# Kernel optimization log

Hardware: AMD Instinct MI355X
Metric: run time of the kernel (lower is better)

The kernel has to match this reference:

```python
import jax, jax.numpy as jnp
import numpy as np

B = 16384
IN = 512
A = 16
E = 9  # 9 position-specific experts
H1, H2, H3 = 512, 256, 128


def setup_inputs() -> dict:
    key = jax.random.key(0)
    ks = jax.random.split(key, 10)
    s = lambda fan_in: 1.0 / np.sqrt(fan_in)
    return {
        "x": jax.random.normal(ks[0], (B, IN), dtype=jnp.float32),
        "position": jax.random.randint(ks[1], (B,), 0, 9, dtype=jnp.int64),
        # torch Linear convention: W [out, in], y = x @ W.T + b; stacked per expert [E, out, in]
        "W1": jax.random.uniform(ks[2], (E, H1, IN), jnp.float32, -s(IN), s(IN)),
        "b1": jax.random.uniform(ks[3], (E, H1), jnp.float32, -s(IN), s(IN)),
        "W2": jax.random.uniform(ks[4], (E, H2, H1), jnp.float32, -s(H1), s(H1)),
        "b2": jax.random.uniform(ks[5], (E, H2), jnp.float32, -s(H1), s(H1)),
        "W3": jax.random.uniform(ks[6], (E, H3, H2), jnp.float32, -s(H2), s(H2)),
        "b3": jax.random.uniform(ks[7], (E, H3), jnp.float32, -s(H2), s(H2)),
        "W4": jax.random.uniform(ks[8], (E, A, H3), jnp.float32, -s(H3), s(H3)),
        "b4": jax.random.uniform(ks[9], (E, A), jnp.float32, -s(H3), s(H3)),
    }


def reference(x, position, W1, b1, W2, b2, W3, b3, W4, b4):
    # Each sample i is routed through expert min(position[i], 8).
    # Dense MoE reference: run all 9 experts over the full batch, then
    # select the routed expert's logits per sample (same math as the
    # per-sample Python loop in the original module).
    pos = jnp.minimum(position, 8)
    h = jax.nn.relu(jnp.einsum('bi,eoi->ebo', x, W1) + b1[:, None, :])   # [E,B,H1]
    h = jax.nn.relu(jnp.einsum('ebi,eoi->ebo', h, W2) + b2[:, None, :])  # [E,B,H2]
    h = jax.nn.relu(jnp.einsum('ebi,eoi->ebo', h, W3) + b3[:, None, :])  # [E,B,H3]
    logits_all = jnp.einsum('ebi,eoi->ebo', h, W4) + b4[:, None, :]      # [E,B,A]
    logits = logits_all[pos, jnp.arange(x.shape[0])]                     # [B,A]
    return jax.nn.softmax(logits, axis=1)
```

## Files before the change

### kernel.cpp

```cpp
#include <hip/hip_runtime.h>

typedef _Float16 f16;
typedef __attribute__((ext_vector_type(8))) _Float16 f16x8;
typedef __attribute__((ext_vector_type(4))) _Float16 f16x4;
typedef __attribute__((ext_vector_type(4))) float f32x4;

#define MFMA16(a, b, c) __builtin_amdgcn_mfma_f32_16x16x32_f16(a, b, c, 0, 0, 0)

#define B_N 16384
#define E_N 9
#define TILE 32
#define NTILE_MAX 520
#define THREADS 512

#define D_IN 512
#define D_H1 512
#define D_H2 256
#define D_H3 128
#define D_A 16

#define O1B 0
#define O2B 4718592
#define O3B 7077888
#define O4B 7667712
#define WPL_BYTES 7704576
#define WSLOTS (WPL_BYTES / 16)

#define IDX_OFF 64
#define WP_OFF 131584
#define WS_NEED (WP_OFF + (size_t)WPL_BYTES)

#define XS_OFF 0
#define H1_OFF 32768
#define H2_OFF 0
#define H3_OFF 16384
#define LDS_BYTES 65536


__global__ void k_bucket(const int* __restrict__ pos, int* __restrict__ hdr,
                         int* __restrict__ idx) {
  __shared__ int cnt[E_N], cur[E_N];
  __shared__ int flag_s;
  const int t = threadIdx.x;
  if (t < E_N) cnt[t] = 0;
  if (t == 0) {
    int nz = 0;
    for (int i = 0; i < 64; ++i) nz |= pos[2 * i + 1];
    flag_s = (nz == 0) ? 1 : 0;
  }
  __syncthreads();
  const bool f64 = flag_s != 0;
  int e[16];
#pragma unroll
  for (int k = 0; k < 16; ++k) {
    int i = k * 1024 + t;
    long long v = f64 ? ((const long long*)pos)[i] : (long long)pos[i];
    v = v < 0 ? 0 : (v > 8 ? 8 : v);
    e[k] = (int)v;
    atomicAdd(&cnt[e[k]], 1);
  }
  __syncthreads();
  if (t == 0) {
    int acc = 0;
    for (int ee = 0; ee < E_N; ++ee) { cur[ee] = acc; acc += cnt[ee]; }
  }
  if (t < E_N) hdr[8 + t] = cnt[t];
  __syncthreads();
#pragma unroll
  for (int k = 0; k < 16; ++k) {
    int i = k * 1024 + t;
    int slot = atomicAdd(&cur[e[k]], 1);
    idx[slot] = i;
  }
}


__global__ void k_wcvt(const float* __restrict__ W1, const float* __restrict__ W2,
                       const float* __restrict__ W3, const float* __restrict__ W4,
                       char* __restrict__ wp) {
  int slot = blockIdx.x * 256 + threadIdx.x;
  if (slot >= WSLOTS) return;
  long addr = (long)slot << 4;
  int lane = (int)((addr >> 4) & 63);
  int lg = lane >> 4, ln = lane & 15;
  const float* src;
  if (addr < O2B) {
    int rec = (int)(addr >> 10);
    int f = rec & 63, w = (rec >> 6) & 7, e = rec >> 9;
    int n = w * 64 + (f >> 5) * 32 + (f & 1) * 16 + ln;
    int k = ((f >> 2) & 7) * 64 + ((f >> 1) & 1) * 32 + lg * 8;
    src = W1 + ((long)e * D_H1 + n) * D_IN + k;
  } else if (addr < O3B) {
    int rec = (int)((addr - O2B) >> 10);
    int f = rec & 31, w = (rec >> 5) & 7, e = rec >> 8;
    int n = w * 32 + (f & 1) * 16 + ln;
    int k = (f >> 2) * 64 + ((f >> 1) & 1) * 32 + lg * 8;
    src = W2 + ((long)e * D_H2 + n) * D_H1 + k;
  } else if (addr < O4B) {
    int rec = (int)((addr - O3B) >> 10);
    int f = rec & 7, w = (rec >> 3) & 7, e = rec >> 6;
    int n = w * 16 + ln;
    int k = (f >> 1) * 64 + (f & 1) * 32 + lg * 8;
    src = W3 + ((long)e * D_H3 + n) * D_H2 + k;
  } else {
    long rel = addr - O4B;
    int e = (int)(rel >> 12);
    int r2 = (int)(rel & 4095);
    int s = r2 >> 4, n = s >> 4, k16 = s & 15;
    src = W4 + ((long)e * D_A + n) * D_H3 + k16 * 8;
  }
  float4 a = *(const float4*)src;
  float4 b = *(const float4*)(src + 4);
  f16x8 h;
  h[0] = (f16)a.x; h[1] = (f16)a.y; h[2] = (f16)a.z; h[3] = (f16)a.w;
  h[4] = (f16)b.x; h[5] = (f16)b.y; h[6] = (f16)b.z; h[7] = (f16)b.w;
  *(f16x8*)(wp + addr) = h;
}


__device__ __forceinline__ f16x8 afrag(const char* base, int strideB, int rowoff,
                                       int kbytes, int lane) {
  int m = rowoff + (lane & 15);
  int q = kbytes + ((lane >> 4) * 16);
  return *(const f16x8*)(base + m * strideB + (q ^ ((lane & 15) << 4)));
}

__device__ __forceinline__ void ldfrag4(f16x8* q, const char* wb, int f0, int lane) {
  const char* p = wb + (long)f0 * 1024 + lane * 16;
  q[0] = *(const f16x8*)(p);
  q[1] = *(const f16x8*)(p + 1024);
  q[2] = *(const f16x8*)(p + 2048);
  q[3] = *(const f16x8*)(p + 3072);
}
__device__ __forceinline__ void ldfrag2(f16x8* q, const char* wb, int f0, int lane) {
  const char* p = wb + (long)f0 * 1024 + lane * 16;
  q[0] = *(const f16x8*)(p);
  q[1] = *(const f16x8*)(p + 1024);
}

__launch_bounds__(THREADS, 4)
__global__ void k_mlp(const float* __restrict__ x,
                      const float* __restrict__ b1, const float* __restrict__ b2,
                      const float* __restrict__ b3, const float* __restrict__ b4,
                      const int* __restrict__ hdr, const int* __restrict__ idx,
                      const char* __restrict__ wp, float* __restrict__ out) {
  __shared__ __align__(16) char lds[LDS_BYTES];

  int b = blockIdx.x;
  int bswz = (b & 7) * (NTILE_MAX / 8) + (b >> 3);

  const int* counts = hdr + 8;
  int e = -1, tile = 0, base = 0, ne = 0;
  {
    int acc = 0, off = 0;
    for (int ee = 0; ee < E_N; ++ee) {
      int n = counts[ee];
      int nt = (n + TILE - 1) / TILE;
      if (bswz < acc + nt) { e = ee; tile = bswz - acc; ne = n; base = off; break; }
      acc += nt; off += n;
    }
  }
  if (e < 0) return;
  const int rvalid = min(TILE, ne - tile * TILE);
  const int row0 = base + tile * TILE;

  const int t = threadIdx.x;
  const int lane = t & 63;
  const int wid = t >> 6;
  const int lg = lane >> 4;
  const int ln = lane & 15;

  const char* wb1 = wp + O1B + (((long)e * 8 + wid) << 16);
  const char* wb2 = wp + O2B + (((long)e * 8 + wid) << 15);
  const char* wb3 = wp + O3B + (((long)e * 8 + wid) << 13);
  const char* wpe4 = wp + O4B + (long)e * 4096;

  f16x8 Q[3][4];
  ldfrag4(Q[0], wb1, 0, lane);
  ldfrag4(Q[1], wb1, 4, lane);

  const float4* x4 = (const float4*)x;
  for (int u = t; u < TILE * (D_IN / 4); u += THREADS) {
    int s = u >> 7, c4 = u & 127;
    float4 v = make_float4(0.f, 0.f, 0.f, 0.f);
    if (s < rvalid) v = x4[(long)idx[row0 + s] * (D_IN / 4) + c4];
    f16x4 h;
    h[0] = (f16)v.x; h[1] = (f16)v.y; h[2] = (f16)v.z; h[3] = (f16)v.w;
    *(f16x4*)(lds + XS_OFF + s * 1024 + ((c4 * 8) ^ ((s & 15) << 4))) = h;
  }
  __syncthreads();

  {
    f32x4 acc[2][2];
#pragma unroll
    for (int g = 0; g < 16; ++g) {
      if (g < 14) ldfrag4(Q[(g + 2) % 3], wb1, (g + 2) * 4, lane);
      const int kb = g & 7;
      if (kb == 0) {
#pragma unroll
        for (int m = 0; m < 2; ++m)
#pragma unroll
          for (int nf = 0; nf < 2; ++nf) acc[m][nf] = (f32x4){0.f, 0.f, 0.f, 0.f};
      }
      f16x8* cq = Q[g % 3];
      __builtin_amdgcn_s_setprio(1);
#pragma unroll
      for (int kc = 0; kc < 2; ++kc) {
        f16x8 A0 = afrag(lds + XS_OFF, 1024, 0, kb * 128 + kc * 64, lane);
        f16x8 A1 = afrag(lds + XS_OFF, 1024, 16, kb * 128 + kc * 64, lane);
        acc[0][0] = MFMA16(A0, cq[kc * 2 + 0], acc[0][0]);
        acc[0][1] = MFMA16(A0, cq[kc * 2 + 1], acc[0][1]);
        acc[1][0] = MFMA16(A1, cq[kc * 2 + 0], acc[1][0]);
        acc[1][1] = MFMA16(A1, cq[kc * 2 + 1], acc[1][1]);
      }
      __builtin_amdgcn_s_setprio(0);
      if (kb == 7) {
        const int nf32 = g >> 3;
#pragma unroll
        for (int nf = 0; nf < 2; ++nf) {
          int n = wid * 64 + nf32 * 32 + nf * 16 + ln;
          float bias = b1[e * D_H1 + n];
#pragma unroll
          for (int m = 0; m < 2; ++m)
#pragma unroll
            for (int j = 0; j < 4; ++j) {
              float v = acc[m][nf][j] + bias;
              v = v > 0.f ? v : 0.f;
              int rw = m * 16 + lg * 4 + j;
              *(f16*)(lds + H1_OFF + rw * 1024 + ((n * 2) ^ ((rw & 15) << 4))) = (f16)v;
            }
        }
      }
    }
  }
  __syncthreads();

  {
    ldfrag4(Q[0], wb2, 0, lane);
    ldfrag4(Q[1], wb2, 4, lane);
    f32x4 acc[2][2];
#pragma unroll
    for (int m = 0; m < 2; ++m)
#pragma unroll
      for (int nf = 0; nf < 2; ++nf) acc[m][nf] = (f32x4){0.f, 0.f, 0.f, 0.f};
#pragma unroll
    for (int g = 0; g < 8; ++g) {
      if (g < 6) ldfrag4(Q[(g + 2) % 3], wb2, (g + 2) * 4, lane);
      f16x8* cq = Q[g % 3];
      __builtin_amdgcn_s_setprio(1);
#pragma unroll
      for (int kc = 0; kc < 2; ++kc) {
        f16x8 A0 = afrag(lds + H1_OFF, 1024, 0, g * 128 + kc * 64, lane);
        f16x8 A1 = afrag(lds + H1_OFF, 1024, 16, g * 128 + kc * 64, lane);
        acc[0][0] = MFMA16(A0, cq[kc * 2 + 0], acc[0][0]);
        acc[0][1] = MFMA16(A0, cq[kc * 2 + 1], acc[0][1]);
        acc[1][0] = MFMA16(A1, cq[kc * 2 + 0], acc[1][0]);
        acc[1][1] = MFMA16(A1, cq[kc * 2 + 1], acc[1][1]);
      }
      __builtin_amdgcn_s_setprio(0);
    }
#pragma unroll
    for (int nf = 0; nf < 2; ++nf) {
      int n = wid * 32 + nf * 16 + ln;
      float bias = b2[e * D_H2 + n];
#pragma unroll
      for (int m = 0; m < 2; ++m)
#pragma unroll
        for (int j = 0; j < 4; ++j) {
          float v = acc[m][nf][j] + bias;
          v = v > 0.f ? v : 0.f;
          int rw = m * 16 + lg * 4 + j;
          *(f16*)(lds + H2_OFF + rw * 512 + ((n * 2) ^ ((rw & 15) << 4))) = (f16)v;
        }
    }
  }
  __syncthreads();

  {
    ldfrag2(Q[0], wb3, 0, lane);
    ldfrag2(Q[1], wb3, 2, lane);
    f32x4 acc3[2];
    acc3[0] = (f32x4){0.f, 0.f, 0.f, 0.f};
    acc3[1] = (f32x4){0.f, 0.f, 0.f, 0.f};
#pragma unroll
    for (int g = 0; g < 4; ++g) {
      if (g < 2) ldfrag2(Q[(g + 2) % 3], wb3, (g + 2) * 2, lane);
      f16x8* cq = Q[g % 3];
      __builtin_amdgcn_s_setprio(1);
#pragma unroll
      for (int kc = 0; kc < 2; ++kc) {
        f16x8 B0 = cq[kc];
#pragma unroll
        for (int m = 0; m < 2; ++m) {
          f16x8 A = afrag(lds + H2_OFF, 512, m * 16, g * 128 + kc * 64, lane);
          acc3[m] = MFMA16(A, B0, acc3[m]);
        }
      }
      __builtin_amdgcn_s_setprio(0);
    }
    int n = wid * 16 + ln;
    float bias = b3[e * D_H3 + n];
#pragma unroll
    for (int m = 0; m < 2; ++m)
#pragma unroll
      for (int j = 0; j < 4; ++j) {
        float v = acc3[m][j] + bias;
        v = v > 0.f ? v : 0.f;
        int rw = m * 16 + lg * 4 + j;
        *(f16*)(lds + H3_OFF + rw * 256 + ((n * 2) ^ ((rw & 15) << 4))) = (f16)v;
      }
  }
  __syncthreads();

  if (wid < 2) {
    f32x4 a4 = (f32x4){0.f, 0.f, 0.f, 0.f};
#pragma unroll
    for (int kc = 0; kc < 4; ++kc) {
      f16x8 Bv = *(const f16x8*)(wpe4 + ln * 256 + kc * 64 + lg * 16);
      f16x8 Av = afrag(lds + H3_OFF, 256, wid * 16, kc * 64, lane);
      a4 = MFMA16(Av, Bv, a4);
    }
    float bias = b4[e * D_A + ln];
#pragma unroll
    for (int j = 0; j < 4; ++j) {
      float v = a4[j] + bias;
      float mx = v;
      for (int msk = 8; msk >= 1; msk >>= 1) mx = fmaxf(mx, __shfl_xor(mx, msk));
      float pe = expf(v - mx);
      float sm = pe;
      for (int msk = 8; msk >= 1; msk >>= 1) sm += __shfl_xor(sm, msk);
      int rl = wid * 16 + lg * 4 + j;
      if (rl < rvalid) out[(long)idx[row0 + rl] * D_A + ln] = pe / sm;
    }
  }
}


extern "C" void kernel_launch(void* const* d_in, const int* in_sizes, int n_in,
                              void* d_out, int out_size, void* d_ws, size_t ws_size,
                              hipStream_t stream) {
  const float* x  = (const float*)d_in[0];
  const int* pos  = (const int*)d_in[1];
  const float* W1 = (const float*)d_in[2];
  const float* b1 = (const float*)d_in[3];
  const float* W2 = (const float*)d_in[4];
  const float* b2 = (const float*)d_in[5];
  const float* W3 = (const float*)d_in[6];
  const float* b3 = (const float*)d_in[7];
  const float* W4 = (const float*)d_in[8];
  const float* b4 = (const float*)d_in[9];
  float* out = (float*)d_out;

  int* hdr = (int*)d_ws;
  int* idx = hdr + IDX_OFF;
  char* wp = (char*)d_ws + WP_OFF;

  hipLaunchKernelGGL(k_bucket, dim3(1), dim3(1024), 0, stream, pos, hdr, idx);
  hipLaunchKernelGGL(k_wcvt, dim3(WSLOTS / 256), dim3(256), 0, stream,
                     W1, W2, W3, W4, wp);
  hipLaunchKernelGGL(k_mlp, dim3(NTILE_MAX), dim3(THREADS), 0, stream,
                     x, b1, b2, b3, b4, hdr, idx, wp, out);
}
```

Baseline: 64.06 us.

## Merge prep kernels, interleave per-warp weight layout, halve LDS for occupancy

Fuses the bucketing and weight-conversion kernels into a single launch, with block 0 doing the bucketing. The packed weights are relaid per expert and warp so that W1, W2 and W3 fragments for a warp sit contiguously, and they are streamed through a rolling 4-register prefetch instead of the old 3x4 buffer. Hidden activations are held in registers and written back into the reused input LDS region after a barrier, which halves LDS to 32KB, and launch bounds are raised to 8 blocks per CU. The cost is extra barriers and a shallower prefetch window, and the higher occupancy target may force register spills.

After: 89.00 us. 38.9% more time.

```diff
diff --git a/kernel.cpp b/kernel.cpp
--- a/kernel.cpp
+++ b/kernel.cpp
@@ -19,9 +19,7 @@
 #define D_H3 128
 #define D_A 16
 
-#define O1B 0
-#define O2B 4718592
-#define O3B 7077888
+#define RPW 104
 #define O4B 7667712
 #define WPL_BYTES 7704576
 #define WSLOTS (WPL_BYTES / 16)
@@ -31,77 +29,79 @@
 #define WS_NEED (WP_OFF + (size_t)WPL_BYTES)
 
 #define XS_OFF 0
-#define H1_OFF 32768
 #define H2_OFF 0
 #define H3_OFF 16384
-#define LDS_BYTES 65536
-
-
-__global__ void k_bucket(const int* __restrict__ pos, int* __restrict__ hdr,
-                         int* __restrict__ idx) {
-  __shared__ int cnt[E_N], cur[E_N];
-  __shared__ int flag_s;
-  const int t = threadIdx.x;
-  if (t < E_N) cnt[t] = 0;
-  if (t == 0) {
-    int nz = 0;
-    for (int i = 0; i < 64; ++i) nz |= pos[2 * i + 1];
-    flag_s = (nz == 0) ? 1 : 0;
-  }
-  __syncthreads();
-  const bool f64 = flag_s != 0;
-  int e[16];
-#pragma unroll
-  for (int k = 0; k < 16; ++k) {
-    int i = k * 1024 + t;
-    long long v = f64 ? ((const long long*)pos)[i] : (long long)pos[i];
-    v = v < 0 ? 0 : (v > 8 ? 8 : v);
-    e[k] = (int)v;
-    atomicAdd(&cnt[e[k]], 1);
-  }
-  __syncthreads();
-  if (t == 0) {
-    int acc = 0;
-    for (int ee = 0; ee < E_N; ++ee) { cur[ee] = acc; acc += cnt[ee]; }
-  }
-  if (t < E_N) hdr[8 + t] = cnt[t];
-  __syncthreads();
-#pragma unroll
-  for (int k = 0; k < 16; ++k) {
-    int i = k * 1024 + t;
-    int slot = atomicAdd(&cur[e[k]], 1);
-    idx[slot] = i;
-  }
-}
-
-
-__global__ void k_wcvt(const float* __restrict__ W1, const float* __restrict__ W2,
+#define LDS_BYTES 32768
+
+
+__global__ void k_prep(const int* __restrict__ pos,
+                       const float* __restrict__ W1, const float* __restrict__ W2,
                        const float* __restrict__ W3, const float* __restrict__ W4,
+                       int* __restrict__ hdr, int* __restrict__ idx,
                        char* __restrict__ wp) {
-  int slot = blockIdx.x * 256 + threadIdx.x;
+  if (blockIdx.x == 0) {
+    __shared__ int cnt[E_N], cur[E_N];
+    __shared__ int flag_s;
+    const int t = threadIdx.x;
+    if (t < E_N) cnt[t] = 0;
+    if (t == 0) {
+      int nz = 0;
+      for (int i = 0; i < 64; ++i) nz |= pos[2 * i + 1];
+      flag_s = (nz == 0) ? 1 : 0;
+    }
+    __syncthreads();
+    const bool f64 = flag_s != 0;
+#pragma unroll 4
+    for (int k = 0; k < 64; ++k) {
+      int i = k * 256 + t;
+      long long v = f64 ? ((const long long*)pos)[i] : (long long)pos[i];
+      v = v < 0 ? 0 : (v > 8 ? 8 : v);
+      atomicAdd(&cnt[(int)v], 1);
+    }
+    __syncthreads();
+    if (t == 0) {
+      int acc = 0;
+      for (int ee = 0; ee < E_N; ++ee) { cur[ee] = acc; acc += cnt[ee]; }
+    }
+    if (t < E_N) hdr[8 + t] = cnt[t];
+    __syncthreads();
+#pragma unroll 4
+    for (int k = 0; k < 64; ++k) {
+      int i = k * 256 + t;
+      long long v = f64 ? ((const long long*)pos)[i] : (long long)pos[i];
+      v = v < 0 ? 0 : (v > 8 ? 8 : v);
+      int slot = atomicAdd(&cur[(int)v], 1);
+      idx[slot] = i;
+    }
+    return;
+  }
+
+  int slot = (blockIdx.x - 1) * 256 + threadIdx.x;
   if (slot >= WSLOTS) return;
   long addr = (long)slot << 4;
-  int lane = (int)((addr >> 4) & 63);
+  int lane = slot & 63;
   int lg = lane >> 4, ln = lane & 15;
   const float* src;
-  if (addr < O2B) {
+  if (addr < O4B) {
     int rec = (int)(addr >> 10);
-    int f = rec & 63, w = (rec >> 6) & 7, e = rec >> 9;
-    int n = w * 64 + (f >> 5) * 32 + (f & 1) * 16 + ln;
-    int k = ((f >> 2) & 7) * 64 + ((f >> 1) & 1) * 32 + lg * 8;
-    src = W1 + ((long)e * D_H1 + n) * D_IN + k;
-  } else if (addr < O3B) {
-    int rec = (int)((addr - O2B) >> 10);
-    int f = rec & 31, w = (rec >> 5) & 7, e = rec >> 8;
-    int n = w * 32 + (f & 1) * 16 + ln;
-    int k = (f >> 2) * 64 + ((f >> 1) & 1) * 32 + lg * 8;
-    src = W2 + ((long)e * D_H2 + n) * D_H1 + k;
-  } else if (addr < O4B) {
-    int rec = (int)((addr - O3B) >> 10);
-    int f = rec & 7, w = (rec >> 3) & 7, e = rec >> 6;
-    int n = w * 16 + ln;
-    int k = (f >> 1) * 64 + (f & 1) * 32 + lg * 8;
-    src = W3 + ((long)e * D_H3 + n) * D_H2 + k;
+    int f = rec % RPW;
+    int ew = rec / RPW;
+    int w = ew & 7, e = ew >> 3;
+    if (f < 64) {
+      int n = w * 64 + ((f >> 5) & 1) * 32 + (f & 1) * 16 + ln;
+      int k = ((f >> 2) & 7) * 64 + ((f >> 1) & 1) * 32 + lg * 8;
+      src = W1 + ((long)e * D_H1 + n) * D_IN + k;
+    } else if (f < 96) {
+      int j = f - 64;
+      int n = w * 32 + (j & 1) * 16 + ln;
+      int k = (j >> 2) * 64 + ((j >> 1) & 1) * 32 + lg * 8;
+      src = W2 + ((long)e * D_H2 + n) * D_H1 + k;
+    } else {
+      int j = f - 96;
+      int n = w * 16 + ln;
+      int k = (j >> 1) * 64 + (j & 1) * 32 + lg * 8;
+      src = W3 + ((long)e * D_H3 + n) * D_H2 + k;
+    }
   } else {
     long rel = addr - O4B;
     int e = (int)(rel >> 12);
@@ -122,23 +122,14 @@
                                        int kbytes, int lane) {
   int m = rowoff + (lane & 15);
   int q = kbytes + ((lane >> 4) * 16);
-  return *(const f16x8*)(base + m * strideB + (q ^ ((lane & 15) << 4)));
-}
-
-__device__ __forceinline__ void ldfrag4(f16x8* q, const char* wb, int f0, int lane) {
-  const char* p = wb + (long)f0 * 1024 + lane * 16;
-  q[0] = *(const f16x8*)(p);
-  q[1] = *(const f16x8*)(p + 1024);
-  q[2] = *(const f16x8*)(p + 2048);
-  q[3] = *(const f16x8*)(p + 3072);
-}
-__device__ __forceinline__ void ldfrag2(f16x8* q, const char* wb, int f0, int lane) {
-  const char* p = wb + (long)f0 * 1024 + lane * 16;
-  q[0] = *(const f16x8*)(p);
-  q[1] = *(const f16x8*)(p + 1024);
-}
-
-__launch_bounds__(THREADS, 4)
+  return *(const f16x8*)(base + m * strideB + (q ^ ((m & 15) << 4)));
+}
+
+__device__ __forceinline__ f16x8 ldfrag(const char* wb, int f, int lane) {
+  return *(const f16x8*)(wb + (long)f * 1024 + lane * 16);
+}
+
+__launch_bounds__(THREADS, 8)
 __global__ void k_mlp(const float* __restrict__ x,
                       const float* __restrict__ b1, const float* __restrict__ b2,
                       const float* __restrict__ b3, const float* __restrict__ b4,
@@ -170,14 +161,14 @@
   const int lg = lane >> 4;
   const int ln = lane & 15;
 
-  const char* wb1 = wp + O1B + (((long)e * 8 + wid) << 16);
-  const char* wb2 = wp + O2B + (((long)e * 8 + wid) << 15);
-  const char* wb3 = wp + O3B + (((long)e * 8 + wid) << 13);
+  const char* wb = wp + ((long)(e * 8 + wid) * RPW << 10);
   const char* wpe4 = wp + O4B + (long)e * 4096;
 
-  f16x8 Q[3][4];
-  ldfrag4(Q[0], wb1, 0, lane);
-  ldfrag4(Q[1], wb1, 4, lane);
+  f16x8 Q[4];
+  Q[0] = ldfrag(wb, 0, lane);
+  Q[1] = ldfrag(wb, 1, lane);
+  Q[2] = ldfrag(wb, 2, lane);
+  Q[3] = ldfrag(wb, 3, lane);
 
   const float4* x4 = (const float4*)x;
   for (int u = t; u < TILE * (D_IN / 4); u += THREADS) {
@@ -190,44 +181,42 @@
   }
   __syncthreads();
 
+  f16x8 h1r[2][2];
   {
     f32x4 acc[2][2];
 #pragma unroll
     for (int g = 0; g < 16; ++g) {
-      if (g < 14) ldfrag4(Q[(g + 2) % 3], wb1, (g + 2) * 4, lane);
-      const int kb = g & 7;
+      const int kb = g & 7, h = g >> 3;
       if (kb == 0) {
 #pragma unroll
         for (int m = 0; m < 2; ++m)
 #pragma unroll
           for (int nf = 0; nf < 2; ++nf) acc[m][nf] = (f32x4){0.f, 0.f, 0.f, 0.f};
       }
-      f16x8* cq = Q[g % 3];
       __builtin_amdgcn_s_setprio(1);
 #pragma unroll
       for (int kc = 0; kc < 2; ++kc) {
         f16x8 A0 = afrag(lds + XS_OFF, 1024, 0, kb * 128 + kc * 64, lane);
         f16x8 A1 = afrag(lds + XS_OFF, 1024, 16, kb * 128 + kc * 64, lane);
-        acc[0][0] = MFMA16(A0, cq[kc * 2 + 0], acc[0][0]);
-        acc[0][1] = MFMA16(A0, cq[kc * 2 + 1], acc[0][1]);
-        acc[1][0] = MFMA16(A1, cq[kc * 2 + 0], acc[1][0]);
-        acc[1][1] = MFMA16(A1, cq[kc * 2 + 1], acc[1][1]);
+#pragma unroll
+        for (int nf = 0; nf < 2; ++nf) {
+          const int i = g * 4 + kc * 2 + nf;
+          acc[0][nf] = MFMA16(A0, Q[i & 3], acc[0][nf]);
+          acc[1][nf] = MFMA16(A1, Q[i & 3], acc[1][nf]);
+          Q[i & 3] = ldfrag(wb, i + 4, lane);
+        }
       }
       __builtin_amdgcn_s_setprio(0);
       if (kb == 7) {
-        const int nf32 = g >> 3;
 #pragma unroll
         for (int nf = 0; nf < 2; ++nf) {
-          int n = wid * 64 + nf32 * 32 + nf * 16 + ln;
-          float bias = b1[e * D_H1 + n];
+          float bias = b1[e * D_H1 + wid * 64 + h * 32 + nf * 16 + ln];
 #pragma unroll
           for (int m = 0; m < 2; ++m)
 #pragma unroll
             for (int j = 0; j < 4; ++j) {
               float v = acc[m][nf][j] + bias;
-              v = v > 0.f ? v : 0.f;
-              int rw = m * 16 + lg * 4 + j;
-              *(f16*)(lds + H1_OFF + rw * 1024 + ((n * 2) ^ ((rw & 15) << 4))) = (f16)v;
+              h1r[h][m][nf * 4 + j] = (f16)(v > 0.f ? v : 0.f);
             }
         }
       }
@@ -235,9 +224,23 @@
   }
   __syncthreads();
 
+#pragma unroll
+  for (int h = 0; h < 2; ++h)
+#pragma unroll
+    for (int m = 0; m < 2; ++m)
+#pragma unroll
+      for (int nf = 0; nf < 2; ++nf)
+#pragma unroll
+        for (int j = 0; j < 4; ++j) {
+          int rw = m * 16 + lg * 4 + j;
+          int n = wid * 64 + h * 32 + nf * 16 + ln;
+          *(f16*)(lds + XS_OFF + rw * 1024 + ((n * 2) ^ ((rw & 15) << 4))) =
+              h1r[h][m][nf * 4 + j];
+        }
+  __syncthreads();
+
+  f16x8 h2r[2];
   {
-    ldfrag4(Q[0], wb2, 0, lane);
-    ldfrag4(Q[1], wb2, 4, lane);
     f32x4 acc[2][2];
 #pragma unroll
     for (int m = 0; m < 2; ++m)
@@ -245,56 +248,63 @@
       for (int nf = 0; nf < 2; ++nf) acc[m][nf] = (f32x4){0.f, 0.f, 0.f, 0.f};
 #pragma unroll
     for (int g = 0; g < 8; ++g) {
-      if (g < 6) ldfrag4(Q[(g + 2) % 3], wb2, (g + 2) * 4, lane);
-      f16x8* cq = Q[g % 3];
       __builtin_amdgcn_s_setprio(1);
 #pragma unroll
       for (int kc = 0; kc < 2; ++kc) {
-        f16x8 A0 = afrag(lds + H1_OFF, 1024, 0, g * 128 + kc * 64, lane);
-        f16x8 A1 = afrag(lds + H1_OFF, 1024, 16, g * 128 + kc * 64, lane);
-        acc[0][0] = MFMA16(A0, cq[kc * 2 + 0], acc[0][0]);
-        acc[0][1] = MFMA16(A0, cq[kc * 2 + 1], acc[0][1]);
-        acc[1][0] = MFMA16(A1, cq[kc * 2 + 0], acc[1][0]);
-        acc[1][1] = MFMA16(A1, cq[kc * 2 + 1], acc[1][1]);
+        f16x8 A0 = afrag(lds + XS_OFF, 1024, 0, g * 128 + kc * 64, lane);
+        f16x8 A1 = afrag(lds + XS_OFF, 1024, 16, g * 128 + kc * 64, lane);
+#pragma unroll
+        for (int nf = 0; nf < 2; ++nf) {
+          const int i = 64 + g * 4 + kc * 2 + nf;
+          acc[0][nf] = MFMA16(A0, Q[i & 3], acc[0][nf]);
+          acc[1][nf] = MFMA16(A1, Q[i & 3], acc[1][nf]);
+          Q[i & 3] = ldfrag(wb, i + 4, lane);
+        }
       }
       __builtin_amdgcn_s_setprio(0);
     }
 #pragma unroll
     for (int nf = 0; nf < 2; ++nf) {
-      int n = wid * 32 + nf * 16 + ln;
-      float bias = b2[e * D_H2 + n];
+      float bias = b2[e * D_H2 + wid * 32 + nf * 16 + ln];
 #pragma unroll
       for (int m = 0; m < 2; ++m)
 #pragma unroll
         for (int j = 0; j < 4; ++j) {
           float v = acc[m][nf][j] + bias;
-          v = v > 0.f ? v : 0.f;
-          int rw = m * 16 + lg * 4 + j;
-          *(f16*)(lds + H2_OFF + rw * 512 + ((n * 2) ^ ((rw & 15) << 4))) = (f16)v;
-        }
-    }
-  }
+          h2r[m][nf * 4 + j] = (f16)(v > 0.f ? v : 0.f);
+        }
+    }
+  }
+  __syncthreads();
+
+#pragma unroll
+  for (int m = 0; m < 2; ++m)
+#pragma unroll
+    for (int nf = 0; nf < 2; ++nf)
+#pragma unroll
+      for (int j = 0; j < 4; ++j) {
+        int rw = m * 16 + lg * 4 + j;
+        int n = wid * 32 + nf * 16 + ln;
+        *(f16*)(lds + H2_OFF + rw * 512 + ((n * 2) ^ ((rw & 15) << 4))) =
+            h2r[m][nf * 4 + j];
+      }
   __syncthreads();
 
   {
-    ldfrag2(Q[0], wb3, 0, lane);
-    ldfrag2(Q[1], wb3, 2, lane);
     f32x4 acc3[2];
     acc3[0] = (f32x4){0.f, 0.f, 0.f, 0.f};
     acc3[1] = (f32x4){0.f, 0.f, 0.f, 0.f};
 #pragma unroll
     for (int g = 0; g < 4; ++g) {
-      if (g < 2) ldfrag2(Q[(g + 2) % 3], wb3, (g + 2) * 2, lane);
-      f16x8* cq = Q[g % 3];
       __builtin_amdgcn_s_setprio(1);
 #pragma unroll
       for (int kc = 0; kc < 2; ++kc) {
-        f16x8 B0 = cq[kc];
-#pragma unroll
-        for (int m = 0; m < 2; ++m) {
-          f16x8 A = afrag(lds + H2_OFF, 512, m * 16, g * 128 + kc * 64, lane);
-          acc3[m] = MFMA16(A, B0, acc3[m]);
-        }
+        const int i = 96 + g * 2 + kc;
+        f16x8 A0 = afrag(lds + H2_OFF, 512, 0, g * 128 + kc * 64, lane);
+        f16x8 A1 = afrag(lds + H2_OFF, 512, 16, g * 128 + kc * 64, lane);
+        acc3[0] = MFMA16(A0, Q[i & 3], acc3[0]);
+        acc3[1] = MFMA16(A1, Q[i & 3], acc3[1]);
+        if (i < 100) Q[i & 3] = ldfrag(wb, i + 4, lane);
       }
       __builtin_amdgcn_s_setprio(0);
     }
@@ -355,9 +365,8 @@
   int* idx = hdr + IDX_OFF;
   char* wp = (char*)d_ws + WP_OFF;
 
-  hipLaunchKernelGGL(k_bucket, dim3(1), dim3(1024), 0, stream, pos, hdr, idx);
-  hipLaunchKernelGGL(k_wcvt, dim3(WSLOTS / 256), dim3(256), 0, stream,
-                     W1, W2, W3, W4, wp);
+  hipLaunchKernelGGL(k_prep, dim3(1 + WSLOTS / 256), dim3(256), 0, stream,
+                     pos, W1, W2, W3, W4, hdr, idx, wp);
   hipLaunchKernelGGL(k_mlp, dim3(NTILE_MAX), dim3(THREADS), 0, stream,
                      x, b1, b2, b3, b4, hdr, idx, wp, out);
 }
```
